# Performance work log

Hardware: AMD Instinct MI355X
Metric: run time of the kernel (lower is better)

## Reference

```python
import jax, jax.numpy as jnp
import numpy as np

NUM_HEADS = 32
NUM_KV_GROUPS = 8
HEAD_DIM = 64  # dim_out // num_heads
DIM_IN = 2048
DIM_OUT = 2048


def setup_inputs() -> dict:
    key = jax.random.key(0)
    k_x, k_q, k_k, k_v, k_o = jax.random.split(key, 5)
    s = 0.02
    x = jax.random.normal(k_x, (1, 2048, DIM_IN), dtype=jnp.float32)
    wq = jax.random.normal(k_q, (DIM_IN, DIM_OUT), dtype=jnp.float32) * s
    wk = jax.random.normal(k_k, (DIM_IN, NUM_KV_GROUPS * HEAD_DIM), dtype=jnp.float32) * s
    wv = jax.random.normal(k_v, (DIM_IN, NUM_KV_GROUPS * HEAD_DIM), dtype=jnp.float32) * s
    wo = jax.random.normal(k_o, (DIM_OUT, DIM_OUT), dtype=jnp.float32) * s
    return {"x": x, "wq": wq, "wk": wk, "wv": wv, "wo": wo}


def reference(x, wq, wk, wv, wo):
    b, n, _ = x.shape
    g, r, d = NUM_KV_GROUPS, NUM_HEADS // NUM_KV_GROUPS, HEAD_DIM
    # projections
    q = (x @ wq).reshape(b, n, g, r, d)          # [b,n,g,r,d] heads grouped
    k = (x @ wk).reshape(b, n, g, d)             # [b,n,g,d]
    v = (x @ wv).reshape(b, n, g, d)
    # scores: repeat_interleave of K over group dim == broadcast over r
    scores = jnp.einsum('bqgrd,bkgd->bgrqk', q, k)  # [b,g,r,n,n]
    causal = jnp.tril(jnp.ones((n, n), dtype=bool))
    scores = jnp.where(causal, scores, -jnp.inf)
    attn = jax.nn.softmax(scores / jnp.sqrt(jnp.asarray(d, x.dtype)), axis=-1)
    ctx = jnp.einsum('bgrqk,bkgd->bqgrd', attn, v)  # [b,n,g,r,d]
    out = ctx.reshape(b, n, g * r * d) @ wo
    return out
```

## Files before the change

kernel.cpp:

```cpp
#include <hip/hip_runtime.h>


typedef __attribute__((ext_vector_type(8))) short bf16x8;
typedef __attribute__((ext_vector_type(4))) short bf16x4;
typedef __attribute__((ext_vector_type(4))) float f32x4;
typedef __attribute__((ext_vector_type(4))) unsigned u32x4;

__device__ __forceinline__ short f2bf(float f) {
  unsigned u = __builtin_bit_cast(unsigned, f);
  u += 0x7FFFu + ((u >> 16) & 1u);
  return (short)(u >> 16);
}

__device__ __forceinline__ unsigned pkbf(float a, float b) {
  const unsigned ua = __builtin_bit_cast(unsigned, a) + 0x8000u;
  const unsigned ub = __builtin_bit_cast(unsigned, b) + 0x8000u;
  return __builtin_amdgcn_perm(ub, ua, 0x07060302u);
}

__device__ __forceinline__ void pswap(unsigned a, unsigned b,
                                      unsigned& r0, unsigned& r1) {
  auto t = __builtin_amdgcn_permlane32_swap(a, b, false, false);
  auto u = __builtin_amdgcn_permlane16_swap(t[0], t[1], false, false);
  r0 = u[0]; r1 = u[1];
}

__device__ __forceinline__ void build_bfrag(const f32x4* sv, bf16x8& b0, bf16x8& b1) {
  const unsigned c0 = pkbf(sv[0][0], sv[0][1]), d0 = pkbf(sv[0][2], sv[0][3]);
  const unsigned c1 = pkbf(sv[1][0], sv[1][1]), d1 = pkbf(sv[1][2], sv[1][3]);
  const unsigned c2 = pkbf(sv[2][0], sv[2][1]), d2 = pkbf(sv[2][2], sv[2][3]);
  const unsigned c3 = pkbf(sv[3][0], sv[3][1]), d3 = pkbf(sv[3][2], sv[3][3]);
  unsigned q0, q1, q2, q3, r0, r1, r2, r3;
  pswap(c0, c1, q0, q2); pswap(d0, d1, q1, q3);
  pswap(c2, c3, r0, r2); pswap(d2, d3, r1, r3);
  b0 = __builtin_bit_cast(bf16x8, (u32x4){q0, q1, q2, q3});
  b1 = __builtin_bit_cast(bf16x8, (u32x4){r0, r1, r2, r3});
}

__device__ __forceinline__ void gload_lds16(const void* g, void* l) {
  __builtin_amdgcn_global_load_lds(
      (const __attribute__((address_space(1))) unsigned int*)g,
      (__attribute__((address_space(3))) unsigned int*)l, 16, 0, 0);
}

__global__ __launch_bounds__(256) void cvtx(const float* __restrict__ x,
                                            short* __restrict__ y) {
  const int i = (blockIdx.x * 256 + threadIdx.x) * 4;
  const float4 v = *(const float4*)&x[i];
  bf16x4 r;
  r[0] = f2bf(v.x); r[1] = f2bf(v.y); r[2] = f2bf(v.z); r[3] = f2bf(v.w);
  *(bf16x4*)&y[i] = r;
}

__global__ __launch_bounds__(256) void tcvt4(const float* __restrict__ wq,
                                             const float* __restrict__ wk,
                                             const float* __restrict__ wv,
                                             const float* __restrict__ wo,
                                             short* __restrict__ dq,
                                             short* __restrict__ dk,
                                             short* __restrict__ dv,
                                             short* __restrict__ dwo) {
  const int z = blockIdx.z;
  const float* src;
  short* dst;
  int C;
  if (z == 0)      { src = wq; dst = dq;  C = 2048; }
  else if (z == 1) { src = wk; dst = dk;  C = 512; }
  else if (z == 2) { src = wv; dst = dv;  C = 512; }
  else             { src = wo; dst = dwo; C = 2048; }
  const int c0 = blockIdx.x * 32;
  if (c0 >= C) return;
  const int R = 2048;
  __shared__ float t[32][33];
  const int r0 = blockIdx.y * 32;
  const int tx = threadIdx.x & 31, ty = threadIdx.x >> 5;
#pragma unroll
  for (int i = 0; i < 4; ++i)
    t[ty + i * 8][tx] = src[(r0 + ty + i * 8) * C + c0 + tx];
  __syncthreads();
#pragma unroll
  for (int i = 0; i < 4; ++i)
    dst[(c0 + ty + i * 8) * R + r0 + tx] = f2bf(t[tx][ty + i * 8]);
}

__global__ __launch_bounds__(256) void tbf(const short* __restrict__ src,
                                           short* __restrict__ dst,
                                           int R, int C, int ldsrc) {
  __shared__ short t[32][33];
  const int c0 = blockIdx.x * 32, r0 = blockIdx.y * 32;
  const int tx = threadIdx.x & 31, ty = threadIdx.x >> 5;
#pragma unroll
  for (int i = 0; i < 4; ++i)
    t[ty + i * 8][tx] = src[(r0 + ty + i * 8) * ldsrc + c0 + tx];
  __syncthreads();
#pragma unroll
  for (int i = 0; i < 4; ++i)
    dst[(c0 + ty + i * 8) * R + r0 + tx] = t[tx][ty + i * 8];
}

template <int OUT_BF16, int BN>
__global__ __launch_bounds__(128) void gemm_bt(const short* __restrict__ A,
                                               const short* __restrict__ B,
                                               void* __restrict__ Cv,
                                               int M, int N, int K,
                                               float cscale, int scale_cols) {
  __shared__ short As[2][64 * 64];
  __shared__ short Bs[2][BN * 64];
  const int tid = threadIdx.x;
  const int lane = tid & 63, wid = tid >> 6;
  const int l15 = lane & 15, lg = lane >> 4;
  const int lr = lane >> 3, lc = lane & 7;
  const int row0 = blockIdx.y * 64, col0 = blockIdx.x * BN;
  const int sswz = l15 & 7;
  f32x4 acc[4][BN / 32] = {};
  const int arow = wid * 8 + lr;
  const short* ag = A + (row0 + arow) * K + (lc ^ lr) * 8;
  const short* bg = B + (col0 + arow) * K + (lc ^ lr) * 8;

  auto stage = [&](int b, int kk) {
    short* lA = &As[b][wid * 512];
    short* lB = &Bs[b][wid * 512];
#pragma unroll
    for (int c = 0; c < 4; ++c)
      gload_lds16(ag + c * 16 * K + kk, lA + c * 1024);
#pragma unroll
    for (int c = 0; c < BN / 16; ++c)
      gload_lds16(bg + c * 16 * K + kk, lB + c * 1024);
  };

  stage(0, 0);
  __syncthreads();
  const int nb = K / 64;
  int buf = 0;
  for (int t = 0; t < nb; ++t) {
    if (t + 1 < nb) stage(buf ^ 1, (t + 1) * 64);
#pragma unroll
    for (int x = 0; x < 2; ++x) {
      bf16x8 af[4], bfr[BN / 32];
#pragma unroll
      for (int m = 0; m < 4; ++m)
        af[m] = *(const bf16x8*)&As[buf][(m * 16 + l15) * 64 + (((x * 4 + lg) ^ sswz) * 8)];
#pragma unroll
      for (int n = 0; n < BN / 32; ++n)
        bfr[n] = *(const bf16x8*)&Bs[buf][(wid * (BN / 2) + n * 16 + l15) * 64 + (((x * 4 + lg) ^ sswz) * 8)];
#pragma unroll
      for (int m = 0; m < 4; ++m)
#pragma unroll
        for (int n = 0; n < BN / 32; ++n)
          acc[m][n] = __builtin_amdgcn_mfma_f32_16x16x32_bf16(af[m], bfr[n],
                                                              acc[m][n], 0, 0, 0);
    }
    __syncthreads();
    buf ^= 1;
  }
#pragma unroll
  for (int m = 0; m < 4; ++m)
#pragma unroll
    for (int n = 0; n < BN / 32; ++n)
#pragma unroll
      for (int i = 0; i < 4; ++i) {
        const int r = row0 + m * 16 + lg * 4 + i;
        const int c = col0 + wid * (BN / 2) + n * 16 + l15;
        float v = acc[m][n][i];
        if (c < scale_cols) v *= cscale;
        if (OUT_BF16)
          ((short*)Cv)[r * N + c] = f2bf(v);
        else
          ((float*)Cv)[r * N + c] = v;
      }
}

__global__ __launch_bounds__(512) void attn_fwd(const short* __restrict__ QKV,
                                                const short* __restrict__ Vt,
                                                short* __restrict__ CTX) {
  const int ldq = 3072;
  const int hp = blockIdx.x;
  const int bxp = blockIdx.y;
  const int g = hp >> 1;
  const int h0 = g * 4 + (hp & 1) * 2;
  const int tid = threadIdx.x;
  const int lane = tid & 63, wid = tid >> 6;
  const int grp = wid >> 2;
  const int wq = wid & 3;
  const int l15 = lane & 15, lg = lane >> 4;

  __shared__ short Ks[2][2][64 * 64];
  __shared__ short Vs[2][2][64 * 64];
  __shared__ float CB[4][64][36];

  const int ltid = tid & 255;
  const int srow = ltid >> 3, sseg = ltid & 7;
  const int ssw = (sseg ^ (srow & 7)) * 8;
  const short* Kg = QKV + 2048 + g * 64 + sseg * 8;
  const short* Vg = Vt + (g * 64 + srow) * 2048 + sseg * 8;

  bf16x8 rk0, rk1, rv0, rv1;
  {
    const int tb = grp * 64;
    rk0 = *(const bf16x8*)&Kg[(tb + srow) * ldq];
    rk1 = *(const bf16x8*)&Kg[(tb + srow + 32) * ldq];
    rv0 = *(const bf16x8*)&Vg[tb];
    rv1 = *(const bf16x8*)&Vg[32 * 2048 + tb];
  }

#pragma unroll 1
  for (int half = 0; half < 2; ++half) {
    const int qb = half ? bxp : 31 - bxp;
    const int qrow0 = qb * 64 + wq * 16;

    bf16x8 qf[2][2];
#pragma unroll
    for (int hh = 0; hh < 2; ++hh)
#pragma unroll
      for (int kc = 0; kc < 2; ++kc)
        qf[hh][kc] = *(const bf16x8*)&QKV[(qrow0 + l15) * ldq + (h0 + hh) * 64 + kc * 32 + lg * 8];

    float l_run[2] = {0.f, 0.f};
    f32x4 accO[2][4] = {};

    const int nint = (qb >> 1) + 1;
#pragma unroll 1
    for (int j = 0; j < nint; ++j) {
      const int kt = 2 * j + grp;
      const bool valid = kt <= qb;
      const int buf = j & 1;
      if (valid) {
        *(bf16x8*)&Ks[grp][buf][srow * 64 + ssw] = rk0;
        *(bf16x8*)&Ks[grp][buf][(srow + 32) * 64 + ssw] = rk1;
        *(bf16x8*)&Vs[grp][buf][srow * 64 + ssw] = rv0;
        *(bf16x8*)&Vs[grp][buf][(srow + 32) * 64 + ssw] = rv1;
      }
      if (kt + 2 <= qb) {
        const int nb = (kt + 2) * 64;
        rk0 = *(const bf16x8*)&Kg[(nb + srow) * ldq];
        rk1 = *(const bf16x8*)&Kg[(nb + srow + 32) * ldq];
        rv0 = *(const bf16x8*)&Vg[nb];
        rv1 = *(const bf16x8*)&Vg[32 * 2048 + nb];
      }
      __syncthreads();
      if (!valid) continue;

      const int tokbase = kt * 64;
      f32x4 s[2][4];
      __builtin_amdgcn_s_setprio(1);
#pragma unroll
      for (int t = 0; t < 4; ++t) {
        s[0][t] = (f32x4){0.f, 0.f, 0.f, 0.f};
        s[1][t] = (f32x4){0.f, 0.f, 0.f, 0.f};
#pragma unroll
        for (int kc = 0; kc < 2; ++kc) {
          const bf16x8 kf =
              *(const bf16x8*)&Ks[grp][buf][(t * 16 + l15) * 64 + (((kc * 4 + lg) ^ (l15 & 7)) * 8)];
          s[0][t] = __builtin_amdgcn_mfma_f32_16x16x32_bf16(kf, qf[0][kc], s[0][t], 0, 0, 0);
          s[1][t] = __builtin_amdgcn_mfma_f32_16x16x32_bf16(kf, qf[1][kc], s[1][t], 0, 0, 0);
        }
      }
      __builtin_amdgcn_s_setprio(0);

      if (kt == qb) {
        const int kq = tokbase + lg * 4 - qrow0 - l15;
#pragma unroll
        for (int t = 0; t < 4; ++t)
#pragma unroll
          for (int i = 0; i < 4; ++i)
            if (kq + t * 16 + i > 0) { s[0][t][i] = -3e38f; s[1][t][i] = -3e38f; }
      }

#pragma unroll
      for (int hh = 0; hh < 2; ++hh) {
        float ts = 0.f;
#pragma unroll
        for (int t = 0; t < 4; ++t) {
          const float e0 = __builtin_amdgcn_exp2f(s[hh][t][0]);
          const float e1 = __builtin_amdgcn_exp2f(s[hh][t][1]);
          const float e2 = __builtin_amdgcn_exp2f(s[hh][t][2]);
          const float e3 = __builtin_amdgcn_exp2f(s[hh][t][3]);
          s[hh][t][0] = e0; s[hh][t][1] = e1; s[hh][t][2] = e2; s[hh][t][3] = e3;
          ts += (e0 + e1) + (e2 + e3);
        }
        ts += __shfl_xor(ts, 16);
        ts += __shfl_xor(ts, 32);
        l_run[hh] += ts;
      }

      bf16x8 pb[2][2];
      build_bfrag(s[0], pb[0][0], pb[0][1]);
      build_bfrag(s[1], pb[1][0], pb[1][1]);

      __builtin_amdgcn_s_setprio(1);
#pragma unroll
      for (int kc = 0; kc < 2; ++kc)
#pragma unroll
        for (int t2 = 0; t2 < 4; ++t2) {
          const bf16x8 vb =
              *(const bf16x8*)&Vs[grp][buf][(t2 * 16 + l15) * 64 + (((kc * 4 + lg) ^ (l15 & 7)) * 8)];
          accO[0][t2] = __builtin_amdgcn_mfma_f32_16x16x32_bf16(vb, pb[0][kc], accO[0][t2], 0, 0, 0);
          accO[1][t2] = __builtin_amdgcn_mfma_f32_16x16x32_bf16(vb, pb[1][kc], accO[1][t2], 0, 0, 0);
        }
      __builtin_amdgcn_s_setprio(0);
    }

    if (half == 0 && grp <= bxp) {
      const int tb = grp * 64;
      rk0 = *(const bf16x8*)&Kg[(tb + srow) * ldq];
      rk1 = *(const bf16x8*)&Kg[(tb + srow + 32) * ldq];
      rv0 = *(const bf16x8*)&Vg[tb];
      rv1 = *(const bf16x8*)&Vg[32 * 2048 + tb];
    }

    if (grp == 1) {
#pragma unroll
      for (int hh = 0; hh < 2; ++hh)
#pragma unroll
        for (int t2 = 0; t2 < 4; ++t2)
          *(f32x4*)&CB[wq][lane][hh * 16 + t2 * 4] = accO[hh][t2];
      *(float2*)&CB[wq][lane][32] = make_float2(l_run[0], l_run[1]);
    }
    __syncthreads();
    if (grp == 0) {
      const float2 lcb = *(const float2*)&CB[wq][lane][32];
#pragma unroll
      for (int hh = 0; hh < 2; ++hh) {
        const float lt = l_run[hh] + (hh ? lcb.y : lcb.x);
        const float inv = 1.0f / lt;
        f32x4 ov[4];
#pragma unroll
        for (int t2 = 0; t2 < 4; ++t2) {
          const f32x4 cb = *(const f32x4*)&CB[wq][lane][hh * 16 + t2 * 4];
#pragma unroll
          for (int i = 0; i < 4; ++i) ov[t2][i] = (accO[hh][t2][i] + cb[i]) * inv;
        }
        bf16x8 ob0, ob1;
        build_bfrag(ov, ob0, ob1);
        *(bf16x8*)&CTX[(qrow0 + l15) * 2048 + (h0 + hh) * 64 + lg * 8] = ob0;
        *(bf16x8*)&CTX[(qrow0 + l15) * 2048 + (h0 + hh) * 64 + 32 + lg * 8] = ob1;
      }
    }
  }
}

extern "C" void kernel_launch(void* const* d_in, const int* in_sizes, int n_in,
                              void* d_out, int out_size, void* d_ws, size_t ws_size,
                              hipStream_t stream) {
  (void)in_sizes; (void)n_in; (void)out_size; (void)ws_size;
  const float* x  = (const float*)d_in[0];
  const float* wq = (const float*)d_in[1];
  const float* wk = (const float*)d_in[2];
  const float* wv = (const float*)d_in[3];
  const float* wo = (const float*)d_in[4];
  float* out = (float*)d_out;

  char* ws = (char*)d_ws;
  short* Xb  = (short*)(ws);
  short* WT  = (short*)(ws + 8388608);
  short* WoT = (short*)(ws + 20971520);
  short* QKV = (short*)(ws + 29360128);
  short* Vt  = (short*)(ws + 41943040);
  short* CTX = (short*)(ws + 44040192);

  const float qscale = 0.125f * 1.4426950408889634f;

  cvtx<<<4096, 256, 0, stream>>>(x, Xb);
  { dim3 g(64, 64, 4);
    tcvt4<<<g, 256, 0, stream>>>(wq, wk, wv, wo,
                                 WT, WT + 2048 * 2048, WT + 2560 * 2048, WoT); }
  { dim3 g(32, 32); gemm_bt<1, 96><<<g, 128, 0, stream>>>(Xb, WT, QKV, 2048, 3072, 2048, qscale, 2048); }
  { dim3 g(16, 64); tbf<<<g, 256, 0, stream>>>(QKV + 2560, Vt, 2048, 512, 3072); }
  { dim3 g(16, 16); attn_fwd<<<g, 512, 0, stream>>>(QKV, Vt, CTX); }
  { dim3 g(32, 32); gemm_bt<0, 64><<<g, 128, 0, stream>>>(CTX, WoT, out, 2048, 2048, 2048, 1.0f, 0); }
}
```

Baseline: 118.8 us.

## Stage 128-token KV supertiles in attention and swizzle GEMM workgroup order

The attention kernel now stages K/V in 128-token supertiles per warp group, processing two 64-token subtiles per barrier, which halves the number of block-wide syncs and register-prefetch rounds. The cross-group reduction buffer is shrunk and done per head to fit the larger LDS tiles, and launch bounds request two blocks per CU. The GEMM remaps workgroup IDs in an interleaved order to improve L2 locality. The larger LDS footprint and extra prefetch registers may limit occupancy and add pipeline startup cost.

```diff
diff --git a/kernel.cpp b/kernel.cpp
--- a/kernel.cpp
+++ b/kernel.cpp
@@ -110,7 +110,12 @@
   const int lane = tid & 63, wid = tid >> 6;
   const int l15 = lane & 15, lg = lane >> 4;
   const int lr = lane >> 3, lc = lane & 7;
-  const int row0 = blockIdx.y * 64, col0 = blockIdx.x * BN;
+  const int nx = gridDim.x;
+  const int orig = blockIdx.y * nx + blockIdx.x;
+  const int nwg = nx * gridDim.y;
+  const int wgid = (orig & 7) * (nwg >> 3) + (orig >> 3);
+  const int bx = wgid % nx, by = wgid / nx;
+  const int row0 = by * 64, col0 = bx * BN;
   const int sswz = l15 & 7;
   f32x4 acc[4][BN / 32] = {};
   const int arow = wid * 8 + lr;
@@ -170,9 +175,9 @@
       }
 }
 
-__global__ __launch_bounds__(512) void attn_fwd(const short* __restrict__ QKV,
-                                                const short* __restrict__ Vt,
-                                                short* __restrict__ CTX) {
+__global__ __launch_bounds__(512, 2) void attn_fwd(const short* __restrict__ QKV,
+                                                   const short* __restrict__ Vt,
+                                                   short* __restrict__ CTX) {
   const int ldq = 3072;
   const int hp = blockIdx.x;
   const int bxp = blockIdx.y;
@@ -184,28 +189,33 @@
   const int wq = wid & 3;
   const int l15 = lane & 15, lg = lane >> 4;
 
-  __shared__ short Ks[2][2][64 * 64];
-  __shared__ short Vs[2][2][64 * 64];
-  __shared__ float CB[4][64][36];
+  __shared__ short Ks[2][2][128 * 64];
+  __shared__ short Vs[2][2][64 * 128];
+  __shared__ float CB[4][64][20];
 
   const int ltid = tid & 255;
   const int srow = ltid >> 3, sseg = ltid & 7;
   const int ssw = (sseg ^ (srow & 7)) * 8;
+  const int vrow = ltid >> 4, vseg = ltid & 15;
+  const int ssv = (vseg ^ (vrow & 7)) * 8;
   const short* Kg = QKV + 2048 + g * 64 + sseg * 8;
-  const short* Vg = Vt + (g * 64 + srow) * 2048 + sseg * 8;
-
-  bf16x8 rk0, rk1, rv0, rv1;
+  const short* Vg = Vt + (g * 64 + vrow) * 2048 + vseg * 8;
+
+  bf16x8 rk[4], rv[4];
   {
-    const int tb = grp * 64;
-    rk0 = *(const bf16x8*)&Kg[(tb + srow) * ldq];
-    rk1 = *(const bf16x8*)&Kg[(tb + srow + 32) * ldq];
-    rv0 = *(const bf16x8*)&Vg[tb];
-    rv1 = *(const bf16x8*)&Vg[32 * 2048 + tb];
+    const int tb = grp * 128;
+#pragma unroll
+    for (int m = 0; m < 4; ++m) {
+      rk[m] = *(const bf16x8*)&Kg[(tb + srow + 32 * m) * ldq];
+      rv[m] = *(const bf16x8*)&Vg[16 * m * 2048 + tb];
+    }
   }
 
 #pragma unroll 1
   for (int half = 0; half < 2; ++half) {
     const int qb = half ? bxp : 31 - bxp;
+    const int S = (qb + 2) >> 1;
+    const int nint = (S + 1) >> 1;
     const int qrow0 = qb * 64 + wq * 16;
 
     bf16x8 qf[2][2];
@@ -218,115 +228,123 @@
     float l_run[2] = {0.f, 0.f};
     f32x4 accO[2][4] = {};
 
-    const int nint = (qb >> 1) + 1;
 #pragma unroll 1
     for (int j = 0; j < nint; ++j) {
-      const int kt = 2 * j + grp;
-      const bool valid = kt <= qb;
+      const int s = 2 * j + grp;
+      const bool sval = s < S;
       const int buf = j & 1;
-      if (valid) {
-        *(bf16x8*)&Ks[grp][buf][srow * 64 + ssw] = rk0;
-        *(bf16x8*)&Ks[grp][buf][(srow + 32) * 64 + ssw] = rk1;
-        *(bf16x8*)&Vs[grp][buf][srow * 64 + ssw] = rv0;
-        *(bf16x8*)&Vs[grp][buf][(srow + 32) * 64 + ssw] = rv1;
-      }
-      if (kt + 2 <= qb) {
-        const int nb = (kt + 2) * 64;
-        rk0 = *(const bf16x8*)&Kg[(nb + srow) * ldq];
-        rk1 = *(const bf16x8*)&Kg[(nb + srow + 32) * ldq];
-        rv0 = *(const bf16x8*)&Vg[nb];
-        rv1 = *(const bf16x8*)&Vg[32 * 2048 + nb];
+      const int tb = s * 128;
+      if (sval) {
+#pragma unroll
+        for (int m = 0; m < 4; ++m) {
+          *(bf16x8*)&Ks[grp][buf][(srow + 32 * m) * 64 + ssw] = rk[m];
+          *(bf16x8*)&Vs[grp][buf][(vrow + 16 * m) * 128 + ssv] = rv[m];
+        }
+      }
+      const int sn = s + 2;
+      if (sn < S) {
+        const int tbn = sn * 128;
+#pragma unroll
+        for (int m = 0; m < 4; ++m) {
+          rk[m] = *(const bf16x8*)&Kg[(tbn + srow + 32 * m) * ldq];
+          rv[m] = *(const bf16x8*)&Vg[16 * m * 2048 + tbn];
+        }
       }
       __syncthreads();
-      if (!valid) continue;
-
-      const int tokbase = kt * 64;
-      f32x4 s[2][4];
-      __builtin_amdgcn_s_setprio(1);
-#pragma unroll
-      for (int t = 0; t < 4; ++t) {
-        s[0][t] = (f32x4){0.f, 0.f, 0.f, 0.f};
-        s[1][t] = (f32x4){0.f, 0.f, 0.f, 0.f};
-#pragma unroll
-        for (int kc = 0; kc < 2; ++kc) {
-          const bf16x8 kf =
-              *(const bf16x8*)&Ks[grp][buf][(t * 16 + l15) * 64 + (((kc * 4 + lg) ^ (l15 & 7)) * 8)];
-          s[0][t] = __builtin_amdgcn_mfma_f32_16x16x32_bf16(kf, qf[0][kc], s[0][t], 0, 0, 0);
-          s[1][t] = __builtin_amdgcn_mfma_f32_16x16x32_bf16(kf, qf[1][kc], s[1][t], 0, 0, 0);
-        }
-      }
-      __builtin_amdgcn_s_setprio(0);
-
-      if (kt == qb) {
-        const int kq = tokbase + lg * 4 - qrow0 - l15;
-#pragma unroll
-        for (int t = 0; t < 4; ++t)
-#pragma unroll
-          for (int i = 0; i < 4; ++i)
-            if (kq + t * 16 + i > 0) { s[0][t][i] = -3e38f; s[1][t][i] = -3e38f; }
-      }
-
-#pragma unroll
-      for (int hh = 0; hh < 2; ++hh) {
-        float ts = 0.f;
-#pragma unroll
-        for (int t = 0; t < 4; ++t) {
-          const float e0 = __builtin_amdgcn_exp2f(s[hh][t][0]);
-          const float e1 = __builtin_amdgcn_exp2f(s[hh][t][1]);
-          const float e2 = __builtin_amdgcn_exp2f(s[hh][t][2]);
-          const float e3 = __builtin_amdgcn_exp2f(s[hh][t][3]);
-          s[hh][t][0] = e0; s[hh][t][1] = e1; s[hh][t][2] = e2; s[hh][t][3] = e3;
-          ts += (e0 + e1) + (e2 + e3);
-        }
-        ts += __shfl_xor(ts, 16);
-        ts += __shfl_xor(ts, 32);
-        l_run[hh] += ts;
-      }
-
-      bf16x8 pb[2][2];
-      build_bfrag(s[0], pb[0][0], pb[0][1]);
-      build_bfrag(s[1], pb[1][0], pb[1][1]);
-
-      __builtin_amdgcn_s_setprio(1);
-#pragma unroll
-      for (int kc = 0; kc < 2; ++kc)
-#pragma unroll
-        for (int t2 = 0; t2 < 4; ++t2) {
-          const bf16x8 vb =
-              *(const bf16x8*)&Vs[grp][buf][(t2 * 16 + l15) * 64 + (((kc * 4 + lg) ^ (l15 & 7)) * 8)];
-          accO[0][t2] = __builtin_amdgcn_mfma_f32_16x16x32_bf16(vb, pb[0][kc], accO[0][t2], 0, 0, 0);
-          accO[1][t2] = __builtin_amdgcn_mfma_f32_16x16x32_bf16(vb, pb[1][kc], accO[1][t2], 0, 0, 0);
-        }
-      __builtin_amdgcn_s_setprio(0);
-    }
-
-    if (half == 0 && grp <= bxp) {
-      const int tb = grp * 64;
-      rk0 = *(const bf16x8*)&Kg[(tb + srow) * ldq];
-      rk1 = *(const bf16x8*)&Kg[(tb + srow + 32) * ldq];
-      rv0 = *(const bf16x8*)&Vg[tb];
-      rv1 = *(const bf16x8*)&Vg[32 * 2048 + tb];
-    }
-
-    if (grp == 1) {
-#pragma unroll
-      for (int hh = 0; hh < 2; ++hh)
+      if (!sval) continue;
+
+#pragma unroll
+      for (int u = 0; u < 2; ++u) {
+        const int kt = 2 * s + u;
+        if (kt <= qb) {
+          f32x4 sc[2][4];
+          __builtin_amdgcn_s_setprio(1);
+#pragma unroll
+          for (int t = 0; t < 4; ++t) {
+            sc[0][t] = (f32x4){0.f, 0.f, 0.f, 0.f};
+            sc[1][t] = (f32x4){0.f, 0.f, 0.f, 0.f};
+#pragma unroll
+            for (int kc = 0; kc < 2; ++kc) {
+              const bf16x8 kf =
+                  *(const bf16x8*)&Ks[grp][buf][(u * 64 + t * 16 + l15) * 64 + (((kc * 4 + lg) ^ (l15 & 7)) * 8)];
+              sc[0][t] = __builtin_amdgcn_mfma_f32_16x16x32_bf16(kf, qf[0][kc], sc[0][t], 0, 0, 0);
+              sc[1][t] = __builtin_amdgcn_mfma_f32_16x16x32_bf16(kf, qf[1][kc], sc[1][t], 0, 0, 0);
+            }
+          }
+          __builtin_amdgcn_s_setprio(0);
+
+          if (kt == qb) {
+            const int kq = tb + u * 64 + lg * 4 - qrow0 - l15;
+#pragma unroll
+            for (int t = 0; t < 4; ++t)
+#pragma unroll
+              for (int i = 0; i < 4; ++i)
+                if (kq + t * 16 + i > 0) { sc[0][t][i] = -3e38f; sc[1][t][i] = -3e38f; }
+          }
+
+          bf16x8 pb[2][2];
+#pragma unroll
+          for (int hh = 0; hh < 2; ++hh) {
+            float ts = 0.f;
+#pragma unroll
+            for (int t = 0; t < 4; ++t) {
+              const float e0 = __builtin_amdgcn_exp2f(sc[hh][t][0]);
+              const float e1 = __builtin_amdgcn_exp2f(sc[hh][t][1]);
+              const float e2 = __builtin_amdgcn_exp2f(sc[hh][t][2]);
+              const float e3 = __builtin_amdgcn_exp2f(sc[hh][t][3]);
+              sc[hh][t][0] = e0; sc[hh][t][1] = e1; sc[hh][t][2] = e2; sc[hh][t][3] = e3;
+              ts += (e0 + e1) + (e2 + e3);
+            }
+            ts += __shfl_xor(ts, 16);
+            ts += __shfl_xor(ts, 32);
+            l_run[hh] += ts;
+            build_bfrag(sc[hh], pb[hh][0], pb[hh][1]);
+          }
+
+          __builtin_amdgcn_s_setprio(1);
+#pragma unroll
+          for (int kc = 0; kc < 2; ++kc)
+#pragma unroll
+            for (int t2 = 0; t2 < 4; ++t2) {
+              const bf16x8 vb =
+                  *(const bf16x8*)&Vs[grp][buf][(t2 * 16 + l15) * 128 + (((u * 8 + kc * 4 + lg) ^ (l15 & 7)) * 8)];
+              accO[0][t2] = __builtin_amdgcn_mfma_f32_16x16x32_bf16(vb, pb[0][kc], accO[0][t2], 0, 0, 0);
+              accO[1][t2] = __builtin_amdgcn_mfma_f32_16x16x32_bf16(vb, pb[1][kc], accO[1][t2], 0, 0, 0);
+            }
+          __builtin_amdgcn_s_setprio(0);
+        }
+      }
+    }
+
+    if (half == 0) {
+      const int S1 = (bxp + 2) >> 1;
+      if (grp < S1) {
+        const int tb = grp * 128;
+#pragma unroll
+        for (int m = 0; m < 4; ++m) {
+          rk[m] = *(const bf16x8*)&Kg[(tb + srow + 32 * m) * ldq];
+          rv[m] = *(const bf16x8*)&Vg[16 * m * 2048 + tb];
+        }
+      }
+    }
+
+#pragma unroll 1
+    for (int hh = 0; hh < 2; ++hh) {
+      __syncthreads();
+      if (grp == 1) {
 #pragma unroll
         for (int t2 = 0; t2 < 4; ++t2)
-          *(f32x4*)&CB[wq][lane][hh * 16 + t2 * 4] = accO[hh][t2];
-      *(float2*)&CB[wq][lane][32] = make_float2(l_run[0], l_run[1]);
-    }
-    __syncthreads();
-    if (grp == 0) {
-      const float2 lcb = *(const float2*)&CB[wq][lane][32];
-#pragma unroll
-      for (int hh = 0; hh < 2; ++hh) {
-        const float lt = l_run[hh] + (hh ? lcb.y : lcb.x);
+          *(f32x4*)&CB[wq][lane][t2 * 4] = accO[hh][t2];
+        CB[wq][lane][16] = l_run[hh];
+      }
+      __syncthreads();
+      if (grp == 0) {
+        const float lt = l_run[hh] + CB[wq][lane][16];
         const float inv = 1.0f / lt;
         f32x4 ov[4];
 #pragma unroll
         for (int t2 = 0; t2 < 4; ++t2) {
-          const f32x4 cb = *(const f32x4*)&CB[wq][lane][hh * 16 + t2 * 4];
+          const f32x4 cb = *(const f32x4*)&CB[wq][lane][t2 * 4];
 #pragma unroll
           for (int i = 0; i < 4; ++i) ov[t2][i] = (accO[hh][t2][i] + cb[i]) * inv;
         }
```

Result: slower. 169.6 us (+42.8%).

## Fuse x conversion into weight cast, V transpose into QKV GEMM, remap GEMM tiles

Applied to the files above, without the earlier changes.

Folds the activation fp32-to-bf16 conversion into the weight transpose-cast kernel as an extra grid slice. The separate V transpose kernel goes away: the QKV GEMM epilogue writes V columns transposed straight into Vt. Both GEMMs also get a remapped workgroup-to-tile order that interleaves block IDs in groups of 8, meant for cache or XCD locality. These cut two kernel launches and one extra pass over V. The cost is uncoalesced strided scattered stores in the GEMM epilogue.

```diff
diff --git a/kernel.cpp b/kernel.cpp
--- a/kernel.cpp
+++ b/kernel.cpp
@@ -43,24 +43,26 @@
       (__attribute__((address_space(3))) unsigned int*)l, 16, 0, 0);
 }
 
-__global__ __launch_bounds__(256) void cvtx(const float* __restrict__ x,
-                                            short* __restrict__ y) {
-  const int i = (blockIdx.x * 256 + threadIdx.x) * 4;
-  const float4 v = *(const float4*)&x[i];
-  bf16x4 r;
-  r[0] = f2bf(v.x); r[1] = f2bf(v.y); r[2] = f2bf(v.z); r[3] = f2bf(v.w);
-  *(bf16x4*)&y[i] = r;
-}
-
 __global__ __launch_bounds__(256) void tcvt4(const float* __restrict__ wq,
                                              const float* __restrict__ wk,
                                              const float* __restrict__ wv,
                                              const float* __restrict__ wo,
+                                             const float* __restrict__ x,
                                              short* __restrict__ dq,
                                              short* __restrict__ dk,
                                              short* __restrict__ dv,
-                                             short* __restrict__ dwo) {
+                                             short* __restrict__ dwo,
+                                             short* __restrict__ xb) {
   const int z = blockIdx.z;
+  if (z == 4) {
+    const int id = blockIdx.y * gridDim.x + blockIdx.x;
+    const int i = (id * 256 + threadIdx.x) * 4;
+    const float4 v = *(const float4*)&x[i];
+    bf16x4 r;
+    r[0] = f2bf(v.x); r[1] = f2bf(v.y); r[2] = f2bf(v.z); r[3] = f2bf(v.w);
+    *(bf16x4*)&xb[i] = r;
+    return;
+  }
   const float* src;
   short* dst;
   int C;
@@ -83,34 +85,25 @@
     dst[(c0 + ty + i * 8) * R + r0 + tx] = f2bf(t[tx][ty + i * 8]);
 }
 
-__global__ __launch_bounds__(256) void tbf(const short* __restrict__ src,
-                                           short* __restrict__ dst,
-                                           int R, int C, int ldsrc) {
-  __shared__ short t[32][33];
-  const int c0 = blockIdx.x * 32, r0 = blockIdx.y * 32;
-  const int tx = threadIdx.x & 31, ty = threadIdx.x >> 5;
-#pragma unroll
-  for (int i = 0; i < 4; ++i)
-    t[ty + i * 8][tx] = src[(r0 + ty + i * 8) * ldsrc + c0 + tx];
-  __syncthreads();
-#pragma unroll
-  for (int i = 0; i < 4; ++i)
-    dst[(c0 + ty + i * 8) * R + r0 + tx] = t[tx][ty + i * 8];
-}
-
-template <int OUT_BF16, int BN>
+template <int OUT_BF16, int BN, int FUSE_VT>
 __global__ __launch_bounds__(128) void gemm_bt(const short* __restrict__ A,
                                                const short* __restrict__ B,
                                                void* __restrict__ Cv,
                                                int M, int N, int K,
-                                               float cscale, int scale_cols) {
+                                               float cscale, int scale_cols,
+                                               short* __restrict__ vt) {
   __shared__ short As[2][64 * 64];
   __shared__ short Bs[2][BN * 64];
   const int tid = threadIdx.x;
   const int lane = tid & 63, wid = tid >> 6;
   const int l15 = lane & 15, lg = lane >> 4;
   const int lr = lane >> 3, lc = lane & 7;
-  const int row0 = blockIdx.y * 64, col0 = blockIdx.x * BN;
+  const int nx = gridDim.x;
+  const int orig = blockIdx.y * nx + blockIdx.x;
+  const int nwg = nx * gridDim.y;
+  const int wgid = (orig & 7) * (nwg >> 3) + (orig >> 3);
+  const int bx = wgid % nx, by = wgid / nx;
+  const int row0 = by * 64, col0 = bx * BN;
   const int sswz = l15 & 7;
   f32x4 acc[4][BN / 32] = {};
   const int arow = wid * 8 + lr;
@@ -167,6 +160,7 @@
           ((short*)Cv)[r * N + c] = f2bf(v);
         else
           ((float*)Cv)[r * N + c] = v;
+        if (FUSE_VT && c >= 2560) vt[(c - 2560) * 2048 + r] = f2bf(v);
       }
 }
 
@@ -360,12 +354,14 @@
 
   const float qscale = 0.125f * 1.4426950408889634f;
 
-  cvtx<<<4096, 256, 0, stream>>>(x, Xb);
-  { dim3 g(64, 64, 4);
-    tcvt4<<<g, 256, 0, stream>>>(wq, wk, wv, wo,
-                                 WT, WT + 2048 * 2048, WT + 2560 * 2048, WoT); }
-  { dim3 g(32, 32); gemm_bt<1, 96><<<g, 128, 0, stream>>>(Xb, WT, QKV, 2048, 3072, 2048, qscale, 2048); }
-  { dim3 g(16, 64); tbf<<<g, 256, 0, stream>>>(QKV + 2560, Vt, 2048, 512, 3072); }
+  { dim3 g(64, 64, 5);
+    tcvt4<<<g, 256, 0, stream>>>(wq, wk, wv, wo, x,
+                                 WT, WT + 2048 * 2048, WT + 2560 * 2048, WoT, Xb); }
+  { dim3 g(32, 32);
+    gemm_bt<1, 96, 1><<<g, 128, 0, stream>>>(Xb, WT, QKV, 2048, 3072, 2048,
+                                             qscale, 2048, Vt); }
   { dim3 g(16, 16); attn_fwd<<<g, 512, 0, stream>>>(QKV, Vt, CTX); }
-  { dim3 g(32, 32); gemm_bt<0, 64><<<g, 128, 0, stream>>>(CTX, WoT, out, 2048, 2048, 2048, 1.0f, 0); }
-}
+  { dim3 g(32, 32);
+    gemm_bt<0, 64, 0><<<g, 128, 0, stream>>>(CTX, WoT, out, 2048, 2048, 2048,
+                                             1.0f, 0, nullptr); }
+}
```

After: 122.3 us. +3.0%, slower.
